# Optimization experiments

Hardware: AMD Instinct MI355X
Metric: run time of the kernel (lower is better)

Reference implementation:

```python
import jax, jax.numpy as jnp
import numpy as np

B, T, C, H = 2, 2048, 1024, 16
D = C // H
SCALE = 1.0 / np.sqrt(D).astype(np.float32)


def setup_inputs() -> dict:
    key = jax.random.key(0)
    kx, kq, kk, kv, ko = jax.random.split(key, 5)
    s = 1.0 / np.sqrt(C).astype(np.float32)
    return {
        "x": jax.random.normal(kx, (B, T, C), dtype=jnp.float32),
        "wq": jax.random.normal(kq, (C, C), dtype=jnp.float32) * s,
        "wk": jax.random.normal(kk, (C, C), dtype=jnp.float32) * s,
        "wv": jax.random.normal(kv, (C, C), dtype=jnp.float32) * s,
        "wo": jax.random.normal(ko, (C, C), dtype=jnp.float32) * s,
    }


def reference(x, wq, wk, wv, wo):
    # nn.Linear(y) = y @ W.T; weights stored [out, in]
    q = (x @ wq.T).reshape(B, T, H, D).transpose(0, 2, 1, 3)  # [B,H,T,D]
    k = (x @ wk.T).reshape(B, T, H, D).transpose(0, 2, 1, 3)
    v = (x @ wv.T).reshape(B, T, H, D).transpose(0, 2, 1, 3)
    scores = jnp.einsum("bhqd,bhkd->bhqk", q, k) * SCALE  # [B,H,T,T]
    causal = jnp.tril(jnp.ones((T, T), dtype=bool))
    scores = jnp.where(causal, scores, -jnp.inf)
    attn = jax.nn.softmax(scores, axis=-1)
    out = jnp.einsum("bhqk,bhkd->bhqd", attn, v)  # [B,H,T,D]
    out = out.transpose(0, 2, 1, 3).reshape(B, T, C)
    return out @ wo.T
```

## Files before the change

### kernel.cpp

```cpp
#include <hip/hip_runtime.h>
#include <hip/hip_bf16.h>

#define B_ 2
#define T_ 2048
#define C_ 1024
#define H_ 16
#define D_ 64
#define M_ (B_*T_)
#define SCALE_ 0.125f
#define LOG2E_ 1.44269504f
#define NEG_ (-1e30f)
#define THR_ 8.0f

typedef __bf16 bf16;
typedef __bf16 bf16x4 __attribute__((ext_vector_type(4)));
typedef __bf16 bf16x8 __attribute__((ext_vector_type(8)));
typedef float  f32x4  __attribute__((ext_vector_type(4)));

#define XB_ELEMS  ((size_t)M_*C_)
#define W_ELEMS   ((size_t)C_*C_)

__device__ __forceinline__ void glds16(const void* g, void* l) {
  __builtin_amdgcn_global_load_lds((const __attribute__((address_space(1))) void*)g,
                                   (__attribute__((address_space(3))) void*)l,
                                   16, 0, 0);
}

__global__ __launch_bounds__(256)
void cvt5(const float* __restrict__ x,  const float* __restrict__ wq,
          const float* __restrict__ wk, const float* __restrict__ wv,
          const float* __restrict__ wo, bf16* __restrict__ out,
          bf16* __restrict__ wodst) {
  int bid = blockIdx.x;
  const float* src; bf16* dst; size_t off;
  if (bid < 2048)      { src = x;  dst = out;                         off = (size_t)bid*2048; }
  else if (bid < 2560) { src = wq; dst = out + XB_ELEMS;              off = (size_t)(bid-2048)*2048; }
  else if (bid < 3072) { src = wk; dst = out + XB_ELEMS +   W_ELEMS;  off = (size_t)(bid-2560)*2048; }
  else if (bid < 3584) { src = wv; dst = out + XB_ELEMS + 2*W_ELEMS;  off = (size_t)(bid-3072)*2048; }
  else                 { src = wo; dst = wodst;                       off = (size_t)(bid-3584)*2048; }
  size_t i = off + (size_t)threadIdx.x * 8;
  f32x4 lo = *(const f32x4*)(src + i);
  f32x4 hi = *(const f32x4*)(src + i + 4);
  bf16x8 r;
  #pragma unroll
  for (int t = 0; t < 4; ++t) { r[t] = (bf16)lo[t]; r[t+4] = (bf16)hi[t]; }
  *(bf16x8*)(dst + i) = r;
}

template<int OUTMODE>
__global__ __launch_bounds__(256)
void gemm_nt(const bf16* __restrict__ Ab,
             const bf16* __restrict__ W0, const bf16* __restrict__ W1,
             const bf16* __restrict__ W2,
             void* __restrict__ O0v, void* __restrict__ O1v, void* __restrict__ O2v,
             int K) {
  __shared__ __align__(16) bf16 As[128*64];
  __shared__ __align__(16) bf16 Bs[128*64];

  const bf16* W = W0;
  void* Ov = O0v;
  bool vtrans = false;
  float oscale = 1.0f;
  if constexpr (OUTMODE == 0) {
    if (blockIdx.z == 0)      { oscale = SCALE_ * LOG2E_; }
    else if (blockIdx.z == 1) { W = W1; Ov = O1v; }
    else                      { W = W2; Ov = O2v; vtrans = true; }
  }

  const int m0 = blockIdx.y * 128, n0 = blockIdx.x * 128;
  const int tid = threadIdx.x, wid = tid >> 6, lane = tid & 63;
  const int wm = wid >> 1, wn = wid & 1;
  const int l15 = lane & 15, grp = lane >> 4;

  f32x4 acc[4][4] = {};

  const int lr8 = lane >> 3;
  const int lkswz = ((lane & 7) ^ lr8) * 8;
  const bf16* Ag = Ab + (size_t)(m0 + wid*8 + lr8) * K + lkswz;
  const bf16* Bg = W  + (size_t)(n0 + wid*8 + lr8) * K + lkswz;

  const int amRow = wm*64 + l15;
  const int bnRow = wn*64 + l15;
  const int swz = l15 & 7;

  for (int k0 = 0; k0 < K; k0 += 64) {
    __syncthreads();
    #pragma unroll
    for (int c = 0; c < 4; ++c) {
      glds16(Ag + (size_t)(c*32)*K + k0, As + (wid + c*4)*512);
      glds16(Bg + (size_t)(c*32)*K + k0, Bs + (wid + c*4)*512);
    }
    __syncthreads();

    #pragma unroll
    for (int ks = 0; ks < 2; ++ks) {
      const int aslot = ((ks*4 + grp) ^ swz) * 8;
      bf16x8 af[4], bfr[4];
      #pragma unroll
      for (int i = 0; i < 4; ++i) {
        af[i]  = *(const bf16x8*)(As + (amRow + i*16)*64 + aslot);
        bfr[i] = *(const bf16x8*)(Bs + (bnRow + i*16)*64 + aslot);
      }
      __builtin_amdgcn_s_setprio(1);
      #pragma unroll
      for (int i = 0; i < 4; ++i)
        #pragma unroll
        for (int j = 0; j < 4; ++j)
          acc[i][j] = __builtin_amdgcn_mfma_f32_16x16x32_bf16(af[i], bfr[j], acc[i][j], 0, 0, 0);
      __builtin_amdgcn_s_setprio(0);
    }
  }

  const int rBase = m0 + wm*64 + grp * 4;
  const int cBase = n0 + wn*64 + l15;
  #pragma unroll
  for (int fm = 0; fm < 4; ++fm) {
    #pragma unroll
    for (int fn = 0; fn < 4; ++fn) {
      #pragma unroll
      for (int j = 0; j < 4; ++j) {
        int m = rBase + fm*16 + j;
        int n = cBase + fn*16;
        if constexpr (OUTMODE == 0) {
          int b = m >> 11, t = m & 2047, h = n >> 6, d = n & 63;
          size_t idx = vtrans ? (((size_t)(b*H_ + h) * D_ + d) * T_ + t)
                              : (((size_t)(b*H_ + h) * T_ + t) * D_ + d);
          ((bf16*)Ov)[idx] = (bf16)(acc[fm][fn][j] * oscale);
        } else {
          ((float*)Ov)[(size_t)m * C_ + n] = acc[fm][fn][j];
        }
      }
    }
  }
}

__global__ __launch_bounds__(256)
void attn_fwd(const bf16* __restrict__ Q, const bf16* __restrict__ Km,
              const bf16* __restrict__ Vt, bf16* __restrict__ Oa) {
  __shared__ __align__(16) bf16 Ks [64*64];
  __shared__ __align__(16) bf16 Vts[64*64];
  __shared__ __align__(16) bf16 Ps [64*64];

  const int id = blockIdx.x;
  const int qt = 31 - (id >> 5);
  const int bh = id & 31;
  const int q0 = qt * 64;
  const int tid = threadIdx.x, wid = tid >> 6, lane = tid & 63;
  const int l15 = lane & 15;
  const int grp = lane >> 4;
  const int myrow4 = grp * 4;
  const int sw = l15 & 7;

  const bf16* Qb = Q  + (size_t)bh * T_ * D_;
  const bf16* Kb = Km + (size_t)bh * T_ * D_;
  const bf16* Vb = Vt + (size_t)bh * D_ * T_;

  const int ksr = tid >> 3, kskc = tid & 7;
  const int wsl = (kskc ^ (ksr & 7)) * 8;
  const int b = bh >> 4, h = bh & 15;

  const int qrow = q0 + wid*16 + l15;
  bf16x8 aq0 = *(const bf16x8*)(Qb + (size_t)qrow*64 +      grp*8);
  bf16x8 aq1 = *(const bf16x8*)(Qb + (size_t)qrow*64 + 32 + grp*8);

  f32x4 oacc[4] = {};
  float m_s = NEG_, l_s = 0.f;

  bf16x8 kv_a = *(const bf16x8*)(Kb + (size_t)(ksr)*64      + kskc*8);
  bf16x8 kv_b = *(const bf16x8*)(Kb + (size_t)(ksr + 32)*64 + kskc*8);
  bf16x8 vt_a = *(const bf16x8*)(Vb + (size_t)(ksr     )*T_ + kskc*8);
  bf16x8 vt_b = *(const bf16x8*)(Vb + (size_t)(ksr + 32)*T_ + kskc*8);

  for (int kt = 0; kt <= qt; ++kt) {
    const int kv0 = kt * 64;

    __syncthreads();
    *(bf16x8*)(Ks  + ksr*64      + wsl) = kv_a;
    *(bf16x8*)(Ks  + (ksr+32)*64 + wsl) = kv_b;
    *(bf16x8*)(Vts + ksr*64      + wsl) = vt_a;
    *(bf16x8*)(Vts + (ksr+32)*64 + wsl) = vt_b;
    __syncthreads();

    {
      const int kn = (kt < qt) ? kv0 + 64 : kv0;
      kv_a = *(const bf16x8*)(Kb + (size_t)(kn + ksr)*64      + kskc*8);
      kv_b = *(const bf16x8*)(Kb + (size_t)(kn + ksr + 32)*64 + kskc*8);
      vt_a = *(const bf16x8*)(Vb + (size_t)(ksr     )*T_ + kn + kskc*8);
      vt_b = *(const bf16x8*)(Vb + (size_t)(ksr + 32)*T_ + kn + kskc*8);
    }

    f32x4 s[4];
    __builtin_amdgcn_s_setprio(1);
    #pragma unroll
    for (int n = 0; n < 4; ++n) {
      int row = n*16 + l15;
      bf16x8 bk0 = *(const bf16x8*)(Ks + row*64 + ((grp     ^ sw)*8));
      bf16x8 bk1 = *(const bf16x8*)(Ks + row*64 + (((grp|4) ^ sw)*8));
      f32x4 a = {};
      a = __builtin_amdgcn_mfma_f32_16x16x32_bf16(bk0, aq0, a, 0, 0, 0);
      a = __builtin_amdgcn_mfma_f32_16x16x32_bf16(bk1, aq1, a, 0, 0, 0);
      s[n] = a;
    }
    __builtin_amdgcn_s_setprio(0);

    float pmax = NEG_;
    if (kt == qt) {
      #pragma unroll
      for (int n = 0; n < 4; ++n)
        #pragma unroll
        for (int j = 0; j < 4; ++j) {
          int kvg = kv0 + n*16 + myrow4 + j;
          float sv = (kvg <= qrow) ? s[n][j] : NEG_;
          s[n][j] = sv;
          pmax = fmaxf(pmax, sv);
        }
    } else {
      #pragma unroll
      for (int n = 0; n < 4; ++n)
        #pragma unroll
        for (int j = 0; j < 4; ++j) pmax = fmaxf(pmax, s[n][j]);
    }
    pmax = fmaxf(pmax, __shfl_xor(pmax, 16));
    pmax = fmaxf(pmax, __shfl_xor(pmax, 32));

    if (__any(pmax > m_s + THR_)) {
      float mnew = fmaxf(m_s, pmax);
      float scold = __builtin_amdgcn_exp2f(m_s - mnew);
      m_s = mnew;
      l_s *= scold;
      #pragma unroll
      for (int j = 0; j < 4; ++j) {
        float scj = __shfl(scold, myrow4 + j);
        #pragma unroll
        for (int n = 0; n < 4; ++n) oacc[n][j] *= scj;
      }
    }

    const int prow = wid*16 + l15;
    float ps = 0.f;
    #pragma unroll
    for (int n = 0; n < 4; ++n) {
      bf16x4 pw;
      #pragma unroll
      for (int j = 0; j < 4; ++j) {
        float p = __builtin_amdgcn_exp2f(s[n][j] - m_s);
        ps += p;
        pw[j] = (bf16)p;
      }
      int sl = (2*n + (grp >> 1)) ^ sw;
      *(bf16x4*)(Ps + prow*64 + sl*8 + (grp & 1)*4) = pw;
    }
    ps += __shfl_xor(ps, 16);
    ps += __shfl_xor(ps, 32);
    l_s += ps;

    asm volatile("s_waitcnt lgkmcnt(0)" ::: "memory");
    __builtin_amdgcn_sched_barrier(0);

    bf16x8 pa0 = *(const bf16x8*)(Ps + prow*64 + ((grp     ^ sw)*8));
    bf16x8 pa1 = *(const bf16x8*)(Ps + prow*64 + (((grp|4) ^ sw)*8));
    __builtin_amdgcn_s_setprio(1);
    #pragma unroll
    for (int n = 0; n < 4; ++n) {
      int vrow = n*16 + l15;
      bf16x8 bv0 = *(const bf16x8*)(Vts + vrow*64 + ((grp     ^ sw)*8));
      bf16x8 bv1 = *(const bf16x8*)(Vts + vrow*64 + (((grp|4) ^ sw)*8));
      oacc[n] = __builtin_amdgcn_mfma_f32_16x16x32_bf16(pa0, bv0, oacc[n], 0, 0, 0);
      oacc[n] = __builtin_amdgcn_mfma_f32_16x16x32_bf16(pa1, bv1, oacc[n], 0, 0, 0);
    }
    __builtin_amdgcn_s_setprio(0);
  }

  const int tg = q0 + wid*16 + myrow4;
  #pragma unroll
  for (int j = 0; j < 4; ++j) {
    float lj = __shfl(l_s, myrow4 + j);
    float inv = 1.f / lj;
    int trow = tg + j;
    #pragma unroll
    for (int n = 0; n < 4; ++n) {
      int ch = h*64 + n*16 + l15;
      Oa[((size_t)(b*T_ + trow)) * C_ + ch] = (bf16)(oacc[n][j] * inv);
    }
  }
}

extern "C" void kernel_launch(void* const* d_in, const int* in_sizes, int n_in,
                              void* d_out, int out_size, void* d_ws, size_t ws_size,
                              hipStream_t stream) {
  const float* x  = (const float*)d_in[0];
  const float* wq = (const float*)d_in[1];
  const float* wk = (const float*)d_in[2];
  const float* wv = (const float*)d_in[3];
  const float* wo = (const float*)d_in[4];

  bf16* q  = (bf16*)d_ws;
  bf16* k  = q  + XB_ELEMS;
  bf16* v  = k  + XB_ELEMS;

  bf16* cvtbuf = (bf16*)d_out;
  bf16* xb  = cvtbuf;
  bf16* wqb = cvtbuf + XB_ELEMS;
  bf16* wkb = wqb + W_ELEMS;
  bf16* wvb = wkb + W_ELEMS;
  bf16* wob_stage = wvb + W_ELEMS;

  const bool bigws = ws_size >= (4*XB_ELEMS + W_ELEMS) * sizeof(bf16);
  bf16* ao  = bigws ? (v + XB_ELEMS) : xb;
  bf16* wob = bigws ? (v + 2*XB_ELEMS) : wob_stage;

  dim3 blk(256);
  cvt5<<<dim3(4096), blk, 0, stream>>>(x, wq, wk, wv, wo, cvtbuf, wob);
  gemm_nt<0><<<dim3(C_/128, M_/128, 3), blk, 0, stream>>>(xb, wqb, wkb, wvb,
                                                          q, k, v, C_);
  attn_fwd<<<dim3(1024), blk, 0, stream>>>(q, k, v, ao);
  bf16* aoSrc = ao;
  if (!bigws) {
    hipMemcpyAsync(q, xb,        XB_ELEMS * sizeof(bf16), hipMemcpyDeviceToDevice, stream);
    hipMemcpyAsync(k, wob_stage, W_ELEMS  * sizeof(bf16), hipMemcpyDeviceToDevice, stream);
    aoSrc = q; wob = k;
  }
  gemm_nt<1><<<dim3(C_/128, M_/128, 1), blk, 0, stream>>>(aoSrc, wob, nullptr, nullptr,
                                                          d_out, nullptr, nullptr, C_);
}
```

Measured before the change: 110.5 us.

## Load K/V MFMA fragments directly from global memory, dropping LDS staging

The attention kernel no longer stages K and V tiles through shared memory with block-wide barriers and register prefetch. Each wave now loads its own MFMA operand fragments straight from global memory, so the two __syncthreads per KV tile and the LDS round trip are gone. The cost is that each of the four waves fetches the same K/V data on its own, relying on L1/L2 to absorb the repeats. It also loses the software prefetch of the next tile, so global load latency may sit on the critical path.

```diff
diff --git a/kernel.cpp b/kernel.cpp
--- a/kernel.cpp
+++ b/kernel.cpp
@@ -137,9 +137,7 @@
 __global__ __launch_bounds__(256)
 void attn_fwd(const bf16* __restrict__ Q, const bf16* __restrict__ Km,
               const bf16* __restrict__ Vt, bf16* __restrict__ Oa) {
-  __shared__ __align__(16) bf16 Ks [64*64];
-  __shared__ __align__(16) bf16 Vts[64*64];
-  __shared__ __align__(16) bf16 Ps [64*64];
+  __shared__ __align__(16) bf16 Ps[64*64];
 
   const int id = blockIdx.x;
   const int qt = 31 - (id >> 5);
@@ -155,53 +153,49 @@
   const bf16* Kb = Km + (size_t)bh * T_ * D_;
   const bf16* Vb = Vt + (size_t)bh * D_ * T_;
 
-  const int ksr = tid >> 3, kskc = tid & 7;
-  const int wsl = (kskc ^ (ksr & 7)) * 8;
   const int b = bh >> 4, h = bh & 15;
 
   const int qrow = q0 + wid*16 + l15;
   bf16x8 aq0 = *(const bf16x8*)(Qb + (size_t)qrow*64 +      grp*8);
   bf16x8 aq1 = *(const bf16x8*)(Qb + (size_t)qrow*64 + 32 + grp*8);
 
+  const bf16* Kf = Kb + (size_t)l15*64 + grp*8;
+  const bf16* Vf = Vb + (size_t)l15*T_ + grp*8;
+
   f32x4 oacc[4] = {};
   float m_s = NEG_, l_s = 0.f;
 
-  bf16x8 kv_a = *(const bf16x8*)(Kb + (size_t)(ksr)*64      + kskc*8);
-  bf16x8 kv_b = *(const bf16x8*)(Kb + (size_t)(ksr + 32)*64 + kskc*8);
-  bf16x8 vt_a = *(const bf16x8*)(Vb + (size_t)(ksr     )*T_ + kskc*8);
-  bf16x8 vt_b = *(const bf16x8*)(Vb + (size_t)(ksr + 32)*T_ + kskc*8);
+  const int prow = wid*16 + l15;
 
   for (int kt = 0; kt <= qt; ++kt) {
     const int kv0 = kt * 64;
 
-    __syncthreads();
-    *(bf16x8*)(Ks  + ksr*64      + wsl) = kv_a;
-    *(bf16x8*)(Ks  + (ksr+32)*64 + wsl) = kv_b;
-    *(bf16x8*)(Vts + ksr*64      + wsl) = vt_a;
-    *(bf16x8*)(Vts + (ksr+32)*64 + wsl) = vt_b;
-    __syncthreads();
-
-    {
-      const int kn = (kt < qt) ? kv0 + 64 : kv0;
-      kv_a = *(const bf16x8*)(Kb + (size_t)(kn + ksr)*64      + kskc*8);
-      kv_b = *(const bf16x8*)(Kb + (size_t)(kn + ksr + 32)*64 + kskc*8);
-      vt_a = *(const bf16x8*)(Vb + (size_t)(ksr     )*T_ + kn + kskc*8);
-      vt_b = *(const bf16x8*)(Vb + (size_t)(ksr + 32)*T_ + kn + kskc*8);
+    bf16x8 bk0[4], bk1[4];
+    #pragma unroll
+    for (int n = 0; n < 4; ++n) {
+      const bf16* kp = Kf + (size_t)(kv0 + n*16)*64;
+      bk0[n] = *(const bf16x8*)(kp);
+      bk1[n] = *(const bf16x8*)(kp + 32);
     }
 
     f32x4 s[4];
     __builtin_amdgcn_s_setprio(1);
     #pragma unroll
     for (int n = 0; n < 4; ++n) {
-      int row = n*16 + l15;
-      bf16x8 bk0 = *(const bf16x8*)(Ks + row*64 + ((grp     ^ sw)*8));
-      bf16x8 bk1 = *(const bf16x8*)(Ks + row*64 + (((grp|4) ^ sw)*8));
       f32x4 a = {};
-      a = __builtin_amdgcn_mfma_f32_16x16x32_bf16(bk0, aq0, a, 0, 0, 0);
-      a = __builtin_amdgcn_mfma_f32_16x16x32_bf16(bk1, aq1, a, 0, 0, 0);
+      a = __builtin_amdgcn_mfma_f32_16x16x32_bf16(bk0[n], aq0, a, 0, 0, 0);
+      a = __builtin_amdgcn_mfma_f32_16x16x32_bf16(bk1[n], aq1, a, 0, 0, 0);
       s[n] = a;
     }
     __builtin_amdgcn_s_setprio(0);
+
+    bf16x8 bv0[4], bv1[4];
+    #pragma unroll
+    for (int n = 0; n < 4; ++n) {
+      const bf16* vp = Vf + (size_t)(n*16)*T_ + kv0;
+      bv0[n] = *(const bf16x8*)(vp);
+      bv1[n] = *(const bf16x8*)(vp + 32);
+    }
 
     float pmax = NEG_;
     if (kt == qt) {
@@ -236,7 +230,6 @@
       }
     }
 
-    const int prow = wid*16 + l15;
     float ps = 0.f;
     #pragma unroll
     for (int n = 0; n < 4; ++n) {
@@ -262,11 +255,8 @@
     __builtin_amdgcn_s_setprio(1);
     #pragma unroll
     for (int n = 0; n < 4; ++n) {
-      int vrow = n*16 + l15;
-      bf16x8 bv0 = *(const bf16x8*)(Vts + vrow*64 + ((grp     ^ sw)*8));
-      bf16x8 bv1 = *(const bf16x8*)(Vts + vrow*64 + (((grp|4) ^ sw)*8));
-      oacc[n] = __builtin_amdgcn_mfma_f32_16x16x32_bf16(pa0, bv0, oacc[n], 0, 0, 0);
-      oacc[n] = __builtin_amdgcn_mfma_f32_16x16x32_bf16(pa1, bv1, oacc[n], 0, 0, 0);
+      oacc[n] = __builtin_amdgcn_mfma_f32_16x16x32_bf16(pa0, bv0[n], oacc[n], 0, 0, 0);
+      oacc[n] = __builtin_amdgcn_mfma_f32_16x16x32_bf16(pa1, bv1[n], oacc[n], 0, 0, 0);
     }
     __builtin_amdgcn_s_setprio(0);
   }
```

After: 211.6 us. +91.4%, slower.

## Double-buffer K/V shared tiles in attention to drop one barrier per step

Applied to the files above, without the earlier changes.

Turns the single K and V shared-memory tiles into ping-pong buffers. The next tile is written into the alternate buffer at the end of each iteration, then the next global prefetch is issued, so only one __syncthreads per iteration remains instead of two. The aim is to cut barrier stalls and overlap the LDS stores with the loop structure. It doubles K/V LDS use, which may lower occupancy, and the prefetch distance stays one tile.

```diff
diff --git a/kernel.cpp b/kernel.cpp
--- a/kernel.cpp
+++ b/kernel.cpp
@@ -137,9 +137,9 @@
 __global__ __launch_bounds__(256)
 void attn_fwd(const bf16* __restrict__ Q, const bf16* __restrict__ Km,
               const bf16* __restrict__ Vt, bf16* __restrict__ Oa) {
-  __shared__ __align__(16) bf16 Ks [64*64];
-  __shared__ __align__(16) bf16 Vts[64*64];
-  __shared__ __align__(16) bf16 Ps [64*64];
+  __shared__ __align__(16) bf16 Kd[2][64*64];
+  __shared__ __align__(16) bf16 Vd[2][64*64];
+  __shared__ __align__(16) bf16 Ps[64*64];
 
   const int id = blockIdx.x;
   const int qt = 31 - (id >> 5);
@@ -170,32 +170,34 @@
   bf16x8 kv_b = *(const bf16x8*)(Kb + (size_t)(ksr + 32)*64 + kskc*8);
   bf16x8 vt_a = *(const bf16x8*)(Vb + (size_t)(ksr     )*T_ + kskc*8);
   bf16x8 vt_b = *(const bf16x8*)(Vb + (size_t)(ksr + 32)*T_ + kskc*8);
+  *(bf16x8*)(Kd[0] + ksr*64      + wsl) = kv_a;
+  *(bf16x8*)(Kd[0] + (ksr+32)*64 + wsl) = kv_b;
+  *(bf16x8*)(Vd[0] + ksr*64      + wsl) = vt_a;
+  *(bf16x8*)(Vd[0] + (ksr+32)*64 + wsl) = vt_b;
+  {
+    const int kn = (qt > 0) ? 64 : 0;
+    kv_a = *(const bf16x8*)(Kb + (size_t)(kn + ksr)*64      + kskc*8);
+    kv_b = *(const bf16x8*)(Kb + (size_t)(kn + ksr + 32)*64 + kskc*8);
+    vt_a = *(const bf16x8*)(Vb + (size_t)(ksr     )*T_ + kn + kskc*8);
+    vt_b = *(const bf16x8*)(Vb + (size_t)(ksr + 32)*T_ + kn + kskc*8);
+  }
+  __syncthreads();
+
+  const int prow = wid*16 + l15;
 
   for (int kt = 0; kt <= qt; ++kt) {
     const int kv0 = kt * 64;
-
-    __syncthreads();
-    *(bf16x8*)(Ks  + ksr*64      + wsl) = kv_a;
-    *(bf16x8*)(Ks  + (ksr+32)*64 + wsl) = kv_b;
-    *(bf16x8*)(Vts + ksr*64      + wsl) = vt_a;
-    *(bf16x8*)(Vts + (ksr+32)*64 + wsl) = vt_b;
-    __syncthreads();
-
-    {
-      const int kn = (kt < qt) ? kv0 + 64 : kv0;
-      kv_a = *(const bf16x8*)(Kb + (size_t)(kn + ksr)*64      + kskc*8);
-      kv_b = *(const bf16x8*)(Kb + (size_t)(kn + ksr + 32)*64 + kskc*8);
-      vt_a = *(const bf16x8*)(Vb + (size_t)(ksr     )*T_ + kn + kskc*8);
-      vt_b = *(const bf16x8*)(Vb + (size_t)(ksr + 32)*T_ + kn + kskc*8);
-    }
+    const int cur = kt & 1;
+    const bf16* Kc = Kd[cur];
+    const bf16* Vc = Vd[cur];
 
     f32x4 s[4];
     __builtin_amdgcn_s_setprio(1);
     #pragma unroll
     for (int n = 0; n < 4; ++n) {
       int row = n*16 + l15;
-      bf16x8 bk0 = *(const bf16x8*)(Ks + row*64 + ((grp     ^ sw)*8));
-      bf16x8 bk1 = *(const bf16x8*)(Ks + row*64 + (((grp|4) ^ sw)*8));
+      bf16x8 bk0 = *(const bf16x8*)(Kc + row*64 + ((grp     ^ sw)*8));
+      bf16x8 bk1 = *(const bf16x8*)(Kc + row*64 + (((grp|4) ^ sw)*8));
       f32x4 a = {};
       a = __builtin_amdgcn_mfma_f32_16x16x32_bf16(bk0, aq0, a, 0, 0, 0);
       a = __builtin_amdgcn_mfma_f32_16x16x32_bf16(bk1, aq1, a, 0, 0, 0);
@@ -236,7 +238,6 @@
       }
     }
 
-    const int prow = wid*16 + l15;
     float ps = 0.f;
     #pragma unroll
     for (int n = 0; n < 4; ++n) {
@@ -263,12 +264,25 @@
     #pragma unroll
     for (int n = 0; n < 4; ++n) {
       int vrow = n*16 + l15;
-      bf16x8 bv0 = *(const bf16x8*)(Vts + vrow*64 + ((grp     ^ sw)*8));
-      bf16x8 bv1 = *(const bf16x8*)(Vts + vrow*64 + (((grp|4) ^ sw)*8));
+      bf16x8 bv0 = *(const bf16x8*)(Vc + vrow*64 + ((grp     ^ sw)*8));
+      bf16x8 bv1 = *(const bf16x8*)(Vc + vrow*64 + (((grp|4) ^ sw)*8));
       oacc[n] = __builtin_amdgcn_mfma_f32_16x16x32_bf16(pa0, bv0, oacc[n], 0, 0, 0);
       oacc[n] = __builtin_amdgcn_mfma_f32_16x16x32_bf16(pa1, bv1, oacc[n], 0, 0, 0);
     }
     __builtin_amdgcn_s_setprio(0);
+
+    if (kt < qt) {
+      *(bf16x8*)(Kd[cur^1] + ksr*64      + wsl) = kv_a;
+      *(bf16x8*)(Kd[cur^1] + (ksr+32)*64 + wsl) = kv_b;
+      *(bf16x8*)(Vd[cur^1] + ksr*64      + wsl) = vt_a;
+      *(bf16x8*)(Vd[cur^1] + (ksr+32)*64 + wsl) = vt_b;
+      const int kn = (kt + 2 <= qt) ? (kv0 + 128) : (kv0 + 64);
+      kv_a = *(const bf16x8*)(Kb + (size_t)(kn + ksr)*64      + kskc*8);
+      kv_b = *(const bf16x8*)(Kb + (size_t)(kn + ksr + 32)*64 + kskc*8);
+      vt_a = *(const bf16x8*)(Vb + (size_t)(ksr     )*T_ + kn + kskc*8);
+      vt_b = *(const bf16x8*)(Vb + (size_t)(ksr + 32)*T_ + kn + kskc*8);
+    }
+    __syncthreads();
   }
 
   const int tg = q0 + wid*16 + myrow4;
```

New measurement: 111.1 us. No clear change (+0.5%).
